# Performance work log

Measured on AMD Instinct MI355X. Metric: run time of the kernel, lower is better.

The kernel has to match this reference:

```python
import jax, jax.numpy as jnp
import numpy as np

B, T, V, E, H = 512, 512, 50000, 100, 40


def gru_dir(x, lens, Wih, Whh, bih, bhh, reverse):
    """One GRU direction with length masking (PyTorch gate math).
    x: [B,T,I]; returns (out [B,T,H] zero-padded past lens, h_last [B,H])."""
    Bx, Tx, _ = x.shape
    Hh = Whh.shape[1]
    # precompute input-side gates: [T,B,3H]
    gx = jnp.einsum('bti,gi->tbg', x, Wih) + bih
    valid = (jnp.arange(Tx)[:, None] < lens[None, :])[..., None]  # [T,B,1]

    def step(h, inputs):
        gx_t, v = inputs
        gh = h @ Whh.T + bhh
        r = jax.nn.sigmoid(gx_t[:, :Hh] + gh[:, :Hh])
        z = jax.nn.sigmoid(gx_t[:, Hh:2 * Hh] + gh[:, Hh:2 * Hh])
        n = jnp.tanh(gx_t[:, 2 * Hh:] + r * gh[:, 2 * Hh:])
        hn = (1.0 - z) * n + z * h
        h = jnp.where(v, hn, h)          # freeze state past valid length
        return h, jnp.where(v, hn, 0.0)  # pad_packed_sequence zero-fills

    h0 = jnp.zeros((Bx, Hh), x.dtype)
    h_last, outs = jax.lax.scan(step, h0, (gx, valid), reverse=reverse)
    return jnp.transpose(outs, (1, 0, 2)), h_last


def setup_inputs() -> dict:
    key = jax.random.key(0)
    ks = jax.random.split(key, 24)
    text_len = jax.random.randint(ks[0], (B,), 1, T + 1)
    text = jax.random.randint(ks[1], (B, T), 1, V)
    text = jnp.where(jnp.arange(T)[None, :] < text_len[:, None], text, 0)
    s = 0.1
    emb = jax.random.normal(ks[2], (V, E), jnp.float32) * s
    emb = emb.at[0].set(0.0)  # padding_idx=0
    def mk(k, shape):
        return jax.random.normal(k, shape, jnp.float32) * s
    inp = {
        'text': text, 'text_len': text_len, 'emb': emb,
        'Wih0f': mk(ks[3], (3 * H, E)), 'Whh0f': mk(ks[4], (3 * H, H)),
        'bih0f': mk(ks[5], (3 * H,)), 'bhh0f': mk(ks[6], (3 * H,)),
        'Wih0b': mk(ks[7], (3 * H, E)), 'Whh0b': mk(ks[8], (3 * H, H)),
        'bih0b': mk(ks[9], (3 * H,)), 'bhh0b': mk(ks[10], (3 * H,)),
        'Wih1f': mk(ks[11], (3 * H, 2 * H)), 'Whh1f': mk(ks[12], (3 * H, H)),
        'bih1f': mk(ks[13], (3 * H,)), 'bhh1f': mk(ks[14], (3 * H,)),
        'Wih1b': mk(ks[15], (3 * H, 2 * H)), 'Whh1b': mk(ks[16], (3 * H, H)),
        'bih1b': mk(ks[17], (3 * H,)), 'bhh1b': mk(ks[18], (3 * H,)),
        'fc1_W': mk(ks[19], (128, 8 * H)), 'fc1_b': mk(ks[20], (128,)),
        'fc2_W': mk(ks[21], (1, 128)), 'fc2_b': mk(ks[22], (1,)),
    }
    return inp


def forward(text, text_len, emb, Wih0f, Whh0f, bih0f, bhh0f, Wih0b, Whh0b, bih0b, bhh0b,
            Wih1f, Whh1f, bih1f, bhh1f, Wih1b, Whh1b, bih1b, bhh1b,
            fc1_W, fc1_b, fc2_W, fc2_b):
    x = emb[text]  # [B,T,E]
    # layer 0 (bidirectional)
    of0, hf0 = gru_dir(x, text_len, Wih0f, Whh0f, bih0f, bhh0f, False)
    ob0, hb0 = gru_dir(x, text_len, Wih0b, Whh0b, bih0b, bhh0b, True)
    x1 = jnp.concatenate([of0, ob0], axis=-1)  # [B,T,2H]; inter-layer dropout is eval no-op
    # layer 1 (bidirectional)
    of1, hf1 = gru_dir(x1, text_len, Wih1f, Whh1f, bih1f, bhh1f, False)
    ob1, hb1 = gru_dir(x1, text_len, Wih1b, Whh1b, bih1b, bhh1b, True)
    out = jnp.concatenate([of1, ob1], axis=-1)  # [B,T,2H], zero past lens
    # masked avg / max pooling over valid timesteps
    avg_pool = jnp.sum(out, axis=1) / text_len[:, None].astype(out.dtype)
    valid = (jnp.arange(T)[None, :] < text_len[:, None])[..., None]  # [B,T,1]
    max_pool = jnp.max(jnp.where(valid, out, -jnp.inf), axis=1)
    # hidden order: [l0_fwd, l0_bwd, l1_fwd, l1_bwd]; cat([-1],[-2],[-3],[-4],...)
    pool_cat = jnp.concatenate([hb1, hf1, hb0, hf0, avg_pool, max_pool], axis=1)  # [B,8H]
    h = pool_cat @ fc1_W.T + fc1_b
    h = jnp.where(h >= 0, h, 0.01 * h)  # leaky_relu (dropouts are eval no-ops)
    return h @ fc2_W.T + fc2_b  # [B,1]


def reference(text, text_len, emb, Wih0f, Whh0f, bih0f, bhh0f, Wih0b, Whh0b, bih0b, bhh0b,
              Wih1f, Whh1f, bih1f, bhh1f, Wih1b, Whh1b, bih1b, bhh1b,
              fc1_W, fc1_b, fc2_W, fc2_b):
    return forward(text, text_len, emb, Wih0f, Whh0f, bih0f, bhh0f, Wih0b, Whh0b, bih0b, bhh0b,
                   Wih1f, Whh1f, bih1f, bhh1f, Wih1b, Whh1b, bih1b, bhh1b,
                   fc1_W, fc1_b, fc2_W, fc2_b)
```

## Files before the change

kernel.cpp:

```cpp
#include <hip/hip_runtime.h>
#include <hip/hip_fp16.h>

#define BB 512
#define TT 512
#define EE 100
#define HH 40
#define GG 120
#define TC 256
#define NC 2
#define NT (TC/64)
#define X1S 96

typedef _Float16 h2_t __attribute__((ext_vector_type(2)));
typedef _Float16 h8_t __attribute__((ext_vector_type(8)));
typedef float    f4_t __attribute__((ext_vector_type(4)));

__device__ __forceinline__ float fdot2_(h2_t a, h2_t b, float c) {
    return __builtin_amdgcn_fdot2(a, b, c, false);
}
__device__ __forceinline__ h2_t pack2_(float x, float y) {
    h2_t r; r[0] = (_Float16)x; r[1] = (_Float16)y; return r;
}
__device__ __forceinline__ float sigmoid_(float x) {
    return __builtin_amdgcn_rcpf(1.0f + __expf(-x));
}
__device__ __forceinline__ float tanhfast_(float x) {
    return 1.0f - 2.0f * __builtin_amdgcn_rcpf(__expf(2.0f * x) + 1.0f);
}

template<int K, bool GATHER>
__global__ __launch_bounds__(256, 1) void fused_kernel(
    const int cg, const int cs, const int nScan,
    const int* __restrict__ text, const __half* __restrict__ emb16,
    const __half* __restrict__ Xh,
    const _Float16* __restrict__ Wt,
    const float* __restrict__ bf, const float* __restrict__ bb,
    __half* __restrict__ gxW, const __half* __restrict__ gxR,
    const _Float16* __restrict__ WhhL,
    const float* __restrict__ bhhF, const float* __restrict__ bhhB,
    const int* __restrict__ lens,
    __half* __restrict__ out0,
    float* __restrict__ hcar, float* __restrict__ hlast,
    float* __restrict__ sumb, float* __restrict__ maxb)
{
    constexpr int KS = (K == 100) ? 4 : 3;
    const int tid = threadIdx.x;

    if ((int)blockIdx.x < nScan) {
        __builtin_amdgcn_s_setprio(3);
        const int wave = tid >> 6, j = tid & 63;
        if (j >= HH) return;
        const int chain = blockIdx.x * 4 + wave;
        const int dir = chain >> 9;
        const int b   = chain & (BB - 1);
        const float* bhh = dir ? bhhB : bhhF;

        h8_t R0,R1,R2,R3,R4, Z0,Z1,Z2,Z3,Z4, N0,N1,N2,N3,N4;
        {
            const _Float16* wr = WhhL + (size_t)dir * 4800;
            const h8_t* pr = (const h8_t*)(wr + (size_t)j * 40);
            const h8_t* pz = (const h8_t*)(wr + (size_t)(40 + j) * 40);
            const h8_t* pn = (const h8_t*)(wr + (size_t)(80 + j) * 40);
            R0=pr[0]; R1=pr[1]; R2=pr[2]; R3=pr[3]; R4=pr[4];
            Z0=pz[0]; Z1=pz[1]; Z2=pz[2]; Z3=pz[3]; Z4=pz[4];
            N0=pn[0]; N1=pn[1]; N2=pn[2]; N3=pn[3]; N4=pn[4];
        }
        asm volatile("" : "+v"(R0),"+v"(R1),"+v"(R2),"+v"(R3),"+v"(R4),
                          "+v"(Z0),"+v"(Z1),"+v"(Z2),"+v"(Z3),"+v"(Z4),
                          "+v"(N0),"+v"(N1),"+v"(N2),"+v"(N3),"+v"(N4));
        const float br = bhh[j], bz = bhh[HH + j], bn = bhh[2*HH + j];
        const int len = lens[b];
        const int chunk = dir ? (NC - 1 - cs) : cs;
        const int tbase = chunk * TC;

        int sBeg, sEnd;
        if (dir == 0) { sBeg = 0; sEnd = min(TC, max(0, len - tbase)); }
        else          { sBeg = max(0, tbase + TC - len); sEnd = TC; }

        float h = (cs == 0) ? 0.0f : hcar[(size_t)(dir * BB + b) * HH + j];
        float psum = 0.0f, pmax = -3.4e38f;
        const size_t gxRow = ((size_t)dir * BB + b) * TC;

        h2_t H0{},H1{},H2{},H3{},H4{},H5{},H6{},H7{},H8{},H9{},
             H10{},H11{},H12{},H13{},H14{},H15{},H16{},H17{},H18{},H19{};
#define RDL(L) __builtin_bit_cast(h2_t, __builtin_amdgcn_readlane(pk_, (L)))
#define REFRESH_H(val) do { \
        const int v_ = (int)__builtin_bit_cast(unsigned short, (_Float16)(val)); \
        const int t_ = __builtin_amdgcn_update_dpp(0, v_, 0x101, 0xf, 0xf, true); \
        const int pk_ = (t_ << 16) | (v_ & 0xffff); \
        H0=RDL(0);  H1=RDL(2);  H2=RDL(4);  H3=RDL(6);  H4=RDL(8); \
        H5=RDL(10); H6=RDL(12); H7=RDL(14); H8=RDL(16); H9=RDL(18); \
        H10=RDL(20); H11=RDL(22); H12=RDL(24); H13=RDL(26); H14=RDL(28); \
        H15=RDL(30); H16=RDL(32); H17=RDL(34); H18=RDL(36); H19=RDL(38); \
} while (0)
        REFRESH_H(h);

        struct G3 { __half r, z, n; };
        auto ldg3 = [&](int sc) -> G3 {
            const int scc = max(0, min(sc, sEnd - 1));
            const int tl = dir ? (TC - 1 - scc) : scc;
            const __half* gp = gxR + (gxRow + tl) * GG;
            G3 g; g.r = gp[j]; g.z = gp[HH + j]; g.n = gp[2*HH + j];
            return g;
        };
#define SL(V,i) __builtin_shufflevector(V, V, 2*(i), 2*(i)+1)
#define DOTQ(Rq,Zq,Nq, A,B,C,D) \
        r0 = fdot2_(SL(Rq,0), (A), r0); \
        z0 = fdot2_(SL(Zq,0), (A), z0); \
        n0 = fdot2_(SL(Nq,0), (A), n0); \
        r1 = fdot2_(SL(Rq,1), (B), r1); \
        z1 = fdot2_(SL(Zq,1), (B), z1); \
        n1 = fdot2_(SL(Nq,1), (B), n1); \
        r0 = fdot2_(SL(Rq,2), (C), r0); \
        z0 = fdot2_(SL(Zq,2), (C), z0); \
        n0 = fdot2_(SL(Nq,2), (C), n0); \
        r1 = fdot2_(SL(Rq,3), (D), r1); \
        z1 = fdot2_(SL(Zq,3), (D), z1); \
        n1 = fdot2_(SL(Nq,3), (D), n1);

        constexpr int PF = 4;
        auto step = [&](int s, G3& g, bool pf) {
            G3 nx;
            if (pf) nx = ldg3(s + PF);
            const int tloc = dir ? (TC - 1 - s) : s;
            float r0 = br, r1 = 0.f, z0 = bz, z1 = 0.f, n0 = bn, n1 = 0.f;
            DOTQ(R0,Z0,N0, H0,H1,H2,H3)
            DOTQ(R1,Z1,N1, H4,H5,H6,H7)
            DOTQ(R2,Z2,N2, H8,H9,H10,H11)
            DOTQ(R3,Z3,N3, H12,H13,H14,H15)
            DOTQ(R4,Z4,N4, H16,H17,H18,H19)
            const float rr = sigmoid_(__half2float(g.r) + r0 + r1);
            const float zz = sigmoid_(__half2float(g.z) + z0 + z1);
            const float nn = tanhfast_(__half2float(g.n) + rr * (n0 + n1));
            const float hn = (1.0f - zz) * nn + zz * h;
            h = hn;
            REFRESH_H(hn);
            if (GATHER) {
                const int t = tbase + tloc;
                out0[((size_t)b * TT + t) * X1S + dir*HH + j] = __float2half(hn);
            } else {
                psum += hn;
                pmax = fmaxf(pmax, hn);
            }
            if (pf) g = nx;
        };

        G3 q0 = {}, q1 = {}, q2 = {}, q3 = {};
        if (sBeg < sEnd) {
            q0 = ldg3(sBeg);
            q1 = ldg3(sBeg + 1);
            q2 = ldg3(sBeg + 2);
            q3 = ldg3(sBeg + 3);
        }
        int s = sBeg;
        for (; s + PF <= sEnd; s += PF) {
            step(s + 0, q0, true);
            step(s + 1, q1, true);
            step(s + 2, q2, true);
            step(s + 3, q3, true);
        }
        if (s     < sEnd) step(s,     q0, false);
        if (s + 1 < sEnd) step(s + 1, q1, false);
        if (s + 2 < sEnd) step(s + 2, q2, false);

        hcar[(size_t)(dir * BB + b) * HH + j] = h;
        const int layer = GATHER ? 0 : 1;
        if (cs == NC - 1)
            hlast[((size_t)(layer * 2 + dir) * BB + b) * HH + j] = h;
        if (!GATHER) {
            const size_t pi = (size_t)b * (2*HH) + dir*HH + j;
            if (cs == 0) { sumb[pi] = psum;  maxb[pi] = pmax; }
            else         { sumb[pi] += psum; maxb[pi] = fmaxf(maxb[pi], pmax); }
        }
        return;
    }

    __builtin_amdgcn_s_setprio(0);
    const int gid = blockIdx.x - nScan;
    const int b    = gid & (BB - 1);
    const int tile = (gid >> 9) & (NT - 1);
    const int dir  = gid >> (9 + 2);
    const int chunk = dir ? (NC - 1 - cg) : cg;
    const int tbase = chunk * TC + tile * 64;
    if (tbase >= lens[b]) return;
    const float* bias = dir ? bb : bf;
    const _Float16* Wg = Wt + (size_t)dir * (KS * 8 * 64 * 8);

    const int w = tid >> 6, l = tid & 63;
    const int row = l & 15, kq = l >> 4;
    const int t0 = tbase + w * 16 + row;
    h8_t A[4];
    if (GATHER) {
        const int tok = text[b * TT + t0];
        const _Float16* ap = (const _Float16*)emb16 + (size_t)tok * 128 + kq * 8;
        #pragma unroll
        for (int ks = 0; ks < KS; ++ks) A[ks] = *(const h8_t*)(ap + ks * 32);
    } else {
        const _Float16* ap = (const _Float16*)Xh + ((size_t)b * TT + t0) * X1S + kq * 8;
        #pragma unroll
        for (int ks = 0; ks < KS; ++ks) A[ks] = *(const h8_t*)(ap + ks * 32);
    }

    f4_t acc[8] = {};
    #pragma unroll
    for (int ks = 0; ks < KS; ++ks)
        #pragma unroll
        for (int f = 0; f < 8; ++f) {
            const h8_t Bf = *(const h8_t*)(Wg + ((size_t)(ks * 8 + f) * 64 + l) * 8);
            acc[f] = __builtin_amdgcn_mfma_f32_16x16x32_f16(A[ks], Bf, acc[f], 0, 0, 0);
        }

    const size_t rowB = ((size_t)dir * BB + b) * TC;
    const int gb = l & 15, rq = l >> 4;
    #pragma unroll
    for (int f = 0; f < 8; ++f) {
        const int gate = f * 16 + gb;
        if (gate < GG) {
            const float bv = bias[gate];
            #pragma unroll
            for (int r = 0; r < 4; ++r) {
                const int tloc = tile * 64 + w * 16 + rq * 4 + r;
                gxW[(rowB + tloc) * GG + gate] = __float2half(acc[f][r] + bv);
            }
        }
    }
}

#define NE2 (50000 * 64)
#define NW0 (2*4*8*64)
#define NW1 (2*3*8*64)
#define NHH (4*120*20)
#define NP0 (BB*TT*8)
__global__ __launch_bounds__(256) void prep_kernel(
    const float* __restrict__ emb,
    const float* __restrict__ Wih0f, const float* __restrict__ Wih0b,
    const float* __restrict__ Wih1f, const float* __restrict__ Wih1b,
    const float* __restrict__ Whh0f, const float* __restrict__ Whh0b,
    const float* __restrict__ Whh1f, const float* __restrict__ Whh1b,
    __half* __restrict__ emb16, _Float16* __restrict__ Wt16,
    _Float16* __restrict__ Whh16, __half* __restrict__ out0)
{
    const int gid = blockIdx.x * 256 + threadIdx.x;
    if (gid < NE2) {
        const int v = gid >> 6, q2 = gid & 63;
        const int k0 = q2 * 2;
        float x0 = 0.f, x1 = 0.f;
        if (k0 < EE) { x0 = emb[(size_t)v * EE + k0]; x1 = emb[(size_t)v * EE + k0 + 1]; }
        ((h2_t*)emb16)[(size_t)v * 64 + q2] = pack2_(x0, x1);
        return;
    }
    int e = gid - NE2;
    if (e < NP0) {
        const int row = e >> 3, q = e & 7;
        ((h2_t*)out0)[(size_t)row * 48 + 40 + q] = pack2_(0.f, 0.f);
        return;
    }
    e -= NP0;
    if (e < NW0) {
        const int l = e & 63, f = (e >> 6) & 7, ks = (e >> 9) & 3, dir = e >> 11;
        const float* W = dir ? Wih0b : Wih0f;
        const int col = f * 16 + (l & 15);
        const int kb  = ks * 32 + (l >> 4) * 8;
        _Float16* dst = Wt16 + (size_t)e * 8;
        #pragma unroll
        for (int i = 0; i < 8; ++i) {
            const int k = kb + i;
            dst[i] = (_Float16)((col < GG && k < EE) ? W[(size_t)col * EE + k] : 0.f);
        }
        return;
    }
    e -= NW0;
    if (e < NW1) {
        const int l = e & 63, f = (e >> 6) & 7;
        const int t = e >> 9;
        const int ks = t % 3, dir = t / 3;
        const float* W = dir ? Wih1b : Wih1f;
        const int col = f * 16 + (l & 15);
        const int kb  = ks * 32 + (l >> 4) * 8;
        _Float16* dst = Wt16 + (size_t)(NW0 + e) * 8;
        #pragma unroll
        for (int i = 0; i < 8; ++i) {
            const int k = kb + i;
            dst[i] = (_Float16)((col < GG && k < 2*HH) ? W[(size_t)col * (2*HH) + k] : 0.f);
        }
        return;
    }
    e -= NW1;
    if (e < NHH) {
        const int ld = e / 2400, rem = e - ld * 2400;
        const int row2 = rem / 20, kk = rem - row2 * 20;
        const float* W = (ld == 0) ? Whh0f : (ld == 1) ? Whh0b
                       : (ld == 2) ? Whh1f : Whh1b;
        ((h2_t*)Whh16)[e] = pack2_(W[row2*HH + 2*kk], W[row2*HH + 2*kk + 1]);
    }
}

__global__ __launch_bounds__(128) void fc_kernel(
    const float* __restrict__ hlast, const float* __restrict__ sumb,
    const float* __restrict__ maxb, const int* __restrict__ lens,
    const float* __restrict__ fc1W, const float* __restrict__ fc1b,
    const float* __restrict__ fc2W, const float* __restrict__ fc2b,
    float* __restrict__ out)
{
    __shared__ float pool[8 * HH];
    __shared__ float red[128];
    const int b = blockIdx.x, tid = threadIdx.x;
    if (tid < HH) {
        pool[tid]        = hlast[(size_t)(3*BB + b) * HH + tid];
        pool[HH + tid]   = hlast[(size_t)(2*BB + b) * HH + tid];
        pool[2*HH + tid] = hlast[(size_t)(1*BB + b) * HH + tid];
        pool[3*HH + tid] = hlast[(size_t)(0*BB + b) * HH + tid];
    }
    const float invLen = 1.0f / (float)lens[b];
    if (tid < 2*HH) {
        pool[4*HH + tid] = sumb[(size_t)b * 2*HH + tid] * invLen;
        pool[6*HH + tid] = maxb[(size_t)b * 2*HH + tid];
    }
    __syncthreads();
    float acc = fc1b[tid];
    for (int k = 0; k < 8*HH; ++k)
        acc = fmaf(pool[k], fc1W[(size_t)tid * (8*HH) + k], acc);
    float v = (acc >= 0.0f) ? acc : 0.01f * acc;
    red[tid] = v * fc2W[tid];
    __syncthreads();
    for (int s = 64; s > 0; s >>= 1) {
        if (tid < s) red[tid] += red[tid + s];
        __syncthreads();
    }
    if (tid == 0) out[b] = red[0] + fc2b[0];
}

extern "C" void kernel_launch(void* const* d_in, const int* in_sizes, int n_in,
                              void* d_out, int out_size, void* d_ws, size_t ws_size,
                              hipStream_t stream) {
    const int*   text  = (const int*)d_in[0];
    const int*   lens  = (const int*)d_in[1];
    const float* emb   = (const float*)d_in[2];
    const float* Wih0f = (const float*)d_in[3];
    const float* Whh0f = (const float*)d_in[4];
    const float* bih0f = (const float*)d_in[5];
    const float* bhh0f = (const float*)d_in[6];
    const float* Wih0b = (const float*)d_in[7];
    const float* Whh0b = (const float*)d_in[8];
    const float* bih0b = (const float*)d_in[9];
    const float* bhh0b = (const float*)d_in[10];
    const float* Wih1f = (const float*)d_in[11];
    const float* Whh1f = (const float*)d_in[12];
    const float* bih1f = (const float*)d_in[13];
    const float* bhh1f = (const float*)d_in[14];
    const float* Wih1b = (const float*)d_in[15];
    const float* Whh1b = (const float*)d_in[16];
    const float* bih1b = (const float*)d_in[17];
    const float* bhh1b = (const float*)d_in[18];
    const float* fc1W  = (const float*)d_in[19];
    const float* fc1b  = (const float*)d_in[20];
    const float* fc2W  = (const float*)d_in[21];
    const float* fc2b  = (const float*)d_in[22];
    float* out = (float*)d_out;

    char* p = (char*)d_ws;
    const size_t gxB = (size_t)2 * BB * TC * GG * sizeof(__half);
    __half* gxb0  = (__half*)p;  p += gxB;
    __half* gxb1  = (__half*)p;  p += gxB;
    __half* out0  = (__half*)p;  p += (size_t)BB * TT * X1S * sizeof(__half);
    float*  hcar  = (float*)p;   p += (size_t)2 * BB * HH * sizeof(float);
    float*  hlast = (float*)p;   p += (size_t)4 * BB * HH * sizeof(float);
    float*  sumb  = (float*)p;   p += (size_t)BB * 2 * HH * sizeof(float);
    float*  maxb  = (float*)p;   p += (size_t)BB * 2 * HH * sizeof(float);
    __half*    emb16 = (__half*)p;    p += (size_t)50000 * 128 * sizeof(__half);
    _Float16*  Wt16  = (_Float16*)p;  p += (size_t)(NW0 + NW1) * 8 * sizeof(_Float16);
    _Float16*  Whh16 = (_Float16*)p;
    __half* gxb[2] = { gxb0, gxb1 };

    const int NG = BB * 2 * NT;
    const int NS = 256;

    {
        const int total = NE2 + NP0 + NW0 + NW1 + NHH;
        prep_kernel<<<(total + 255) / 256, 256, 0, stream>>>(
            emb, Wih0f, Wih0b, Wih1f, Wih1b, Whh0f, Whh0b, Whh1f, Whh1b,
            emb16, Wt16, Whh16, out0);
    }

    fused_kernel<EE, true><<<NG, 256, 0, stream>>>(0, 0, 0,
        text, emb16, nullptr, Wt16, bih0f, bih0b,
        gxb[0], gxb[0], Whh16, bhh0f, bhh0b,
        lens, out0, hcar, hlast, sumb, maxb);
    for (int ci = 1; ci < NC; ++ci)
        fused_kernel<EE, true><<<NS + NG, 256, 0, stream>>>(ci, ci - 1, NS,
            text, emb16, nullptr, Wt16, bih0f, bih0b,
            gxb[ci & 1], gxb[(ci - 1) & 1], Whh16, bhh0f, bhh0b,
            lens, out0, hcar, hlast, sumb, maxb);
    fused_kernel<EE, true><<<NS, 256, 0, stream>>>(0, NC - 1, NS,
        text, emb16, nullptr, Wt16, bih0f, bih0b,
        gxb[0], gxb[(NC - 1) & 1], Whh16, bhh0f, bhh0b,
        lens, out0, hcar, hlast, sumb, maxb);

    fused_kernel<2*HH, false><<<NG, 256, 0, stream>>>(0, 0, 0,
        text, emb16, out0, Wt16 + (size_t)NW0 * 8, bih1f, bih1b,
        gxb[0], gxb[0], Whh16 + 9600, bhh1f, bhh1b,
        lens, out0, hcar, hlast, sumb, maxb);
    for (int ci = 1; ci < NC; ++ci)
        fused_kernel<2*HH, false><<<NS + NG, 256, 0, stream>>>(ci, ci - 1, NS,
            text, emb16, out0, Wt16 + (size_t)NW0 * 8, bih1f, bih1b,
            gxb[ci & 1], gxb[(ci - 1) & 1], Whh16 + 9600, bhh1f, bhh1b,
            lens, out0, hcar, hlast, sumb, maxb);
    fused_kernel<2*HH, false><<<NS, 256, 0, stream>>>(0, NC - 1, NS,
        text, emb16, out0, Wt16 + (size_t)NW0 * 8, bih1f, bih1b,
        gxb[0], gxb[(NC - 1) & 1], Whh16 + 9600, bhh1f, bhh1b,
        lens, out0, hcar, hlast, sumb, maxb);

    fc_kernel<<<BB, 128, 0, stream>>>(hlast, sumb, maxb, lens,
        fc1W, fc1b, fc2W, fc2b, out);
}
```

Measured before the change: 499.1 us.

## Stage precomputed gate rows through LDS in 16-step double-buffered windows

The scan waves no longer issue three scalar global loads per timestep with a 4-step prefetch. Each wave now loads a 16-timestep window of input-gate rows as wide float4 loads into registers, writes them to a per-wave double-buffered LDS stage partway through the current window, and reads each step's gates from LDS one step ahead. This aims to hide global memory latency on the serial recurrence and to coalesce the loads. The cost is added LDS traffic, extra registers for the staged window, and reliance on in-wave ordering with no barriers.

New measurement: 725.1 us. 1.45x slower.

```diff
diff --git a/kernel.cpp b/kernel.cpp
--- a/kernel.cpp
+++ b/kernel.cpp
@@ -44,6 +44,7 @@
     float* __restrict__ sumb, float* __restrict__ maxb)
 {
     constexpr int KS = (K == 100) ? 4 : 3;
+    __shared__ __align__(16) char stg[2][4][4096];
     const int tid = threadIdx.x;
 
     if ((int)blockIdx.x < nScan) {
@@ -96,11 +97,28 @@
         REFRESH_H(h);
 
         struct G3 { __half r, z, n; };
-        auto ldg3 = [&](int sc) -> G3 {
-            const int scc = max(0, min(sc, sEnd - 1));
-            const int tl = dir ? (TC - 1 - scc) : scc;
-            const __half* gp = gxR + (gxRow + tl) * GG;
-            G3 g; g.r = gp[j]; g.z = gp[HH + j]; g.n = gp[2*HH + j];
+        char* myStg0 = &stg[0][wave][0];
+        char* myStg1 = &stg[1][wave][0];
+        auto rowlo = [&](int W) { return dir ? (TC - 16 - W * 16) : (W * 16); };
+        auto issueLoads = [&](int W, float4* L) {
+            const float4* src =
+                (const float4*)((const _Float16*)gxR + (gxRow + rowlo(W)) * GG);
+            #pragma unroll
+            for (int i = 0; i < 6; ++i) L[i] = src[i * 40 + j];
+        };
+        auto writeLds = [&](int W, const float4* L) {
+            char* d = (W & 1) ? myStg1 : myStg0;
+            #pragma unroll
+            for (int i = 0; i < 6; ++i)
+                *(float4*)(d + (i * 40 + j) * 16) = L[i];
+        };
+        auto ldsG3 = [&](int s) -> G3 {
+            const int sc = min(s, sEnd - 1);
+            const int Wx = sc >> 4, ls = sc & 15;
+            const int rl = dir ? (15 - ls) : ls;
+            const __half* hp =
+                (const __half*)(((Wx & 1) ? myStg1 : myStg0) + rl * 240);
+            G3 g; g.r = hp[j]; g.z = hp[HH + j]; g.n = hp[2*HH + j];
             return g;
         };
 #define SL(V,i) __builtin_shufflevector(V, V, 2*(i), 2*(i)+1)
@@ -118,10 +136,11 @@
         z1 = fdot2_(SL(Zq,3), (D), z1); \
         n1 = fdot2_(SL(Nq,3), (D), n1);
 
-        constexpr int PF = 4;
-        auto step = [&](int s, G3& g, bool pf) {
-            G3 nx;
-            if (pf) nx = ldg3(s + PF);
+        G3 g0 = { __half(0.f), __half(0.f), __half(0.f) };
+        auto doStep = [&](int s) {
+            G3 gn_ = g0;
+            const bool pf = (s + 1 < sEnd);
+            if (pf) gn_ = ldsG3(s + 1);
             const int tloc = dir ? (TC - 1 - s) : s;
             float r0 = br, r1 = 0.f, z0 = bz, z1 = 0.f, n0 = bn, n1 = 0.f;
             DOTQ(R0,Z0,N0, H0,H1,H2,H3)
@@ -129,9 +148,9 @@
             DOTQ(R2,Z2,N2, H8,H9,H10,H11)
             DOTQ(R3,Z3,N3, H12,H13,H14,H15)
             DOTQ(R4,Z4,N4, H16,H17,H18,H19)
-            const float rr = sigmoid_(__half2float(g.r) + r0 + r1);
-            const float zz = sigmoid_(__half2float(g.z) + z0 + z1);
-            const float nn = tanhfast_(__half2float(g.n) + rr * (n0 + n1));
+            const float rr = sigmoid_(__half2float(g0.r) + r0 + r1);
+            const float zz = sigmoid_(__half2float(g0.z) + z0 + z1);
+            const float nn = tanhfast_(__half2float(g0.n) + rr * (n0 + n1));
             const float hn = (1.0f - zz) * nn + zz * h;
             h = hn;
             REFRESH_H(hn);
@@ -142,26 +161,25 @@
                 psum += hn;
                 pmax = fmaxf(pmax, hn);
             }
-            if (pf) g = nx;
+            g0 = gn_;
         };
 
-        G3 q0 = {}, q1 = {}, q2 = {}, q3 = {};
         if (sBeg < sEnd) {
-            q0 = ldg3(sBeg);
-            q1 = ldg3(sBeg + 1);
-            q2 = ldg3(sBeg + 2);
-            q3 = ldg3(sBeg + 3);
-        }
-        int s = sBeg;
-        for (; s + PF <= sEnd; s += PF) {
-            step(s + 0, q0, true);
-            step(s + 1, q1, true);
-            step(s + 2, q2, true);
-            step(s + 3, q3, true);
-        }
-        if (s     < sEnd) step(s,     q0, false);
-        if (s + 1 < sEnd) step(s + 1, q1, false);
-        if (s + 2 < sEnd) step(s + 2, q2, false);
+            const int Wbeg = sBeg >> 4, Wend = (sEnd + 15) >> 4;
+            float4 L[6];
+            issueLoads(Wbeg, L);
+            writeLds(Wbeg, L);
+            g0 = ldsG3(sBeg);
+            for (int W = Wbeg; W < Wend; ++W) {
+                const bool more = (W + 1 < Wend);
+                if (more) issueLoads(W + 1, L);
+                const int s0 = max(W * 16, sBeg), s1 = min(W * 16 + 16, sEnd);
+                const int m = (s1 - s0 > 12) ? (s0 + 12) : s0;
+                for (int s = s0; s < m; ++s) doStep(s);
+                if (more) writeLds(W + 1, L);
+                for (int s = m; s < s1; ++s) doStep(s);
+            }
+        }
 
         hcar[(size_t)(dir * BB + b) * HH + j] = h;
         const int layer = GATHER ? 0 : 1;
```
